# Kernel optimization log

Measured on AMD Instinct MI355X. Metric: run time of the kernel, lower is better.

## Reference

```python
import jax, jax.numpy as jnp
import numpy as np

N = 50000      # total nodes in batched graph
E = 800000     # total edges (avg degree 16)
B = 512        # number of graphs in batch
F_IN = 74      # input node feature size
H = 64         # hidden size per layer
OUT = 64       # output_feats
EPS = 1e-5     # BatchNorm eps


def setup_inputs() -> dict:
    key = jax.random.key(0)
    ks = jax.random.split(key, 32)
    d = {}
    d['feats'] = jax.random.normal(ks[0], (N, F_IN), dtype=jnp.float32)
    d['src'] = jax.random.randint(ks[1], (E,), 0, N)
    d['dst'] = jax.random.randint(ks[2], (E,), 0, N)
    d['graph_ids'] = jnp.sort(jax.random.randint(ks[3], (N,), 0, B))
    dims = [F_IN, H, H, H]
    i = 4
    for l in range(3):
        din, dout = dims[l], dims[l + 1]
        d[f'W{l}'] = jax.random.normal(ks[i], (din, dout), jnp.float32) / np.sqrt(din).astype(np.float32); i += 1
        d[f'b{l}'] = jnp.zeros((dout,), jnp.float32)
        d[f'rW{l}'] = jax.random.normal(ks[i], (din, dout), jnp.float32) / np.sqrt(din).astype(np.float32); i += 1
        d[f'rb{l}'] = jnp.zeros((dout,), jnp.float32)
        d[f'g{l}'] = jnp.ones((dout,), jnp.float32)    # BN gamma
        d[f'be{l}'] = jnp.zeros((dout,), jnp.float32)  # BN beta
    d['aw_W'] = jax.random.normal(ks[i], (H, 1), jnp.float32) / np.sqrt(H).astype(np.float32); i += 1
    d['aw_b'] = jnp.zeros((1,), jnp.float32)
    d['out_W'] = jax.random.normal(ks[i], (2 * H, OUT), jnp.float32) / np.sqrt(2 * H).astype(np.float32); i += 1
    d['out_b'] = jnp.zeros((OUT,), jnp.float32)
    return d


def _gcn_layer(x, src, dst, W, b, rW, rb, g, be):
    # GraphConv, norm='none': out = sum-aggregate(X W) + b, then relu
    xw = x @ W                                                    # [N, dout]
    agg = jax.ops.segment_sum(xw[src], dst, num_segments=N) + b   # gather/scatter over edges
    h = jax.nn.relu(agg)
    # residual: relu(Linear(x))
    h = h + jax.nn.relu(x @ rW + rb)
    # dropout p=0 -> identity
    # BatchNorm1d (training-mode batch statistics, biased variance)
    mean = jnp.mean(h, axis=0)
    var = jnp.var(h, axis=0)
    return (h - mean) * jax.lax.rsqrt(var + EPS) * g + be


def reference(feats, src, dst, graph_ids,
              W0, b0, rW0, rb0, g0, be0,
              W1, b1, rW1, rb1, g1, be1,
              W2, b2, rW2, rb2, g2, be2,
              aw_W, aw_b, out_W, out_b):
    h = feats
    h = _gcn_layer(h, src, dst, W0, b0, rW0, rb0, g0, be0)
    h = _gcn_layer(h, src, dst, W1, b1, rW1, rb1, g1, be1)
    h = _gcn_layer(h, src, dst, W2, b2, rW2, rb2, g2, be2)
    # WeightedSumAndMax readout
    w = jax.nn.sigmoid(h @ aw_W + aw_b)                               # [N, 1]
    h_sum = jax.ops.segment_sum(h * w, graph_ids, num_segments=B)     # [B, H]
    h_max = jax.ops.segment_max(h, graph_ids, num_segments=B)         # [B, H]
    h_max = jnp.where(jnp.isfinite(h_max), h_max, 0.0)                # empty graphs -> 0 (dgl max_nodes)
    h_g = jnp.concatenate([h_sum, h_max], axis=1)                     # [B, 2H]
    return h_g @ out_W + out_b                                        # [B, OUT]
```

## Files before the change

### kernel.cpp

```cpp
#include <hip/hip_runtime.h>
#include <hip/hip_bf16.h>
#include <math.h>

#define NN 50000
#define NE 800000
#define NB 512
#define FIN 74
#define HD 64
#define BN_EPS 1e-5f

#define CHUNK 32
#define ELLW 32
#define NBLK ((NN + CHUNK - 1) / CHUNK)
#define NBUCK2 NBLK
#define EB2 128
#define EPB (NE / EB2)
#define OCAPW 96


__global__ __launch_bounds__(256) void hist2_kernel(const int* __restrict__ dst,
                                                    int* __restrict__ H,
                                                    float* __restrict__ stats012,
                                                    unsigned long long* __restrict__ xw_zrow,
                                                    const float* __restrict__ W0,
                                                    const float* __restrict__ rW0,
                                                    float2* __restrict__ Wpk0) {
    __shared__ int lh[NBUCK2];
    int b = blockIdx.x, tid = threadIdx.x;
    for (int i = tid; i < NBUCK2; i += 256) lh[i] = 0;
    __syncthreads();
    int e0 = b * EPB;
    for (int i = tid; i < EPB; i += 256) atomicAdd(&lh[dst[e0 + i] >> 5], 1);
    if (b == 0) {
        for (int i = tid; i < 384; i += 256) stats012[i] = 0.f;
        if (tid < 16) xw_zrow[tid] = 0ull;
        for (int i = tid; i < FIN * HD; i += 256) Wpk0[i] = make_float2(W0[i], rW0[i]);
    }
    __syncthreads();
    for (int i = tid; i < NBUCK2; i += 256) H[b * NBUCK2 + i] = lh[i];
}

__global__ __launch_bounds__(128) void scanA2_kernel(int* __restrict__ H, int* __restrict__ T) {
    __shared__ int l[128];
    int k = blockIdx.x, tid = threadIdx.x;
    int v = H[tid * NBUCK2 + k];
    l[tid] = v;
    __syncthreads();
    for (int off = 1; off < 128; off <<= 1) {
        int t = (tid >= off) ? l[tid - off] : 0;
        __syncthreads();
        l[tid] += t;
        __syncthreads();
    }
    H[tid * NBUCK2 + k] = l[tid] - v;
    if (tid == 127) T[k] = l[127];
}

__global__ __launch_bounds__(256) void scanB2_kernel(const int* __restrict__ T,
                                                     int* __restrict__ bbase) {
    __shared__ int l[256];
    __shared__ int carry;
    int tid = threadIdx.x;
    if (tid == 0) carry = 0;
    __syncthreads();
    for (int c0 = 0; c0 < NBUCK2; c0 += 256) {
        int v = (c0 + tid < NBUCK2) ? T[c0 + tid] : 0;
        l[tid] = v;
        __syncthreads();
        for (int off = 1; off < 256; off <<= 1) {
            int t = (tid >= off) ? l[tid - off] : 0;
            __syncthreads();
            l[tid] += t;
            __syncthreads();
        }
        if (c0 + tid < NBUCK2) bbase[c0 + tid] = l[tid] - v + carry;
        __syncthreads();
        if (tid == 0) carry += l[255];
        __syncthreads();
    }
    if (tid == 0) bbase[NBUCK2] = carry;
}

__global__ __launch_bounds__(256) void scatter2_kernel(const int* __restrict__ src,
                                                       const int* __restrict__ dst,
                                                       const int* __restrict__ H,
                                                       const int* __restrict__ bbase,
                                                       unsigned* __restrict__ pairs) {
    __shared__ int cur[NBUCK2];
    int b = blockIdx.x, tid = threadIdx.x;
    for (int i = tid; i < NBUCK2; i += 256) cur[i] = H[b * NBUCK2 + i] + bbase[i];
    __syncthreads();
    int e0 = b * EPB;
    for (int i = tid; i < EPB; i += 256) {
        int d = dst[e0 + i];
        int s = src[e0 + i];
        int pos = atomicAdd(&cur[d >> 5], 1);
        pairs[pos] = (unsigned)s | ((unsigned)(d & 31) << 17);
    }
}


template <int K>
__global__ __launch_bounds__(256) void gemm_dual_kernel(
    const float* __restrict__ x, const float2* __restrict__ Wpk,
    const float* __restrict__ rb, __hip_bfloat16* __restrict__ xw,
    __hip_bfloat16* __restrict__ res, int n) {
    __shared__ float2 sW[K * HD];
    __shared__ float srb[64];
    for (int i = threadIdx.x; i < K * HD; i += 256) sW[i] = Wpk[i];
    if (threadIdx.x < 64) srb[threadIdx.x] = rb[threadIdx.x];
    __syncthreads();
    int wl = threadIdx.x >> 6, lane = threadIdx.x & 63;
    for (int r0 = (blockIdx.x * 4 + wl) * 8; r0 < n; r0 += gridDim.x * 32) {
        float a1[8], a2[8];
#pragma unroll
        for (int r = 0; r < 8; ++r) { a1[r] = 0.f; a2[r] = 0.f; }
#pragma unroll
        for (int c0 = 0; c0 < K; c0 += 64) {
            const int cl = (K - c0 < 64) ? (K - c0) : 64;
            float xv[8];
#pragma unroll
            for (int r = 0; r < 8; ++r) {
                int row = r0 + r;
                xv[r] = (lane < cl && row < n) ? x[(size_t)row * K + c0 + lane] : 0.f;
            }
            for (int j = 0; j < cl; ++j) {
                float2 w = sW[(c0 + j) * HD + lane];
#pragma unroll
                for (int r = 0; r < 8; ++r) {
                    float xb = __uint_as_float(
                        __builtin_amdgcn_readlane(__float_as_uint(xv[r]), j));
                    a1[r] = fmaf(xb, w.x, a1[r]);
                    a2[r] = fmaf(xb, w.y, a2[r]);
                }
            }
        }
#pragma unroll
        for (int r = 0; r < 8; ++r) {
            int row = r0 + r;
            if (row < n) {
                xw[(size_t)row * HD + lane] = __float2bfloat16(a1[r]);
                res[(size_t)row * HD + lane] = __float2bfloat16(fmaxf(a2[r] + srb[lane], 0.f));
            }
        }
    }
}

__global__ void fold_kernel(const float* __restrict__ stats, const float* __restrict__ g,
                            const float* __restrict__ be, const float* __restrict__ W,
                            const float* __restrict__ rW, const float* __restrict__ rb,
                            float2* __restrict__ Wpk, float* __restrict__ shiftW,
                            float* __restrict__ rbp) {
    __shared__ float sc[64], sh[64];
    int t = threadIdx.x;
    if (t < 64) {
        float mean = stats[t] / (float)NN;
        float var = stats[64 + t] / (float)NN - mean * mean;
        float scale = g[t] * rsqrtf(var + BN_EPS);
        sc[t] = scale;
        sh[t] = be[t] - mean * scale;
    }
    __syncthreads();
    for (int i = t; i < 64 * 64; i += 256) {
        int k = i >> 6;
        Wpk[i] = make_float2(sc[k] * W[i], sc[k] * rW[i]);
    }
    if (t < 64) {
        float sw = 0.f, srw = 0.f;
        for (int k = 0; k < 64; ++k) {
            sw = fmaf(sh[k], W[k * 64 + t], sw);
            srw = fmaf(sh[k], rW[k * 64 + t], srw);
        }
        shiftW[t] = sw;
        rbp[t] = rb[t] + srw;
    }
}

__device__ __forceinline__ float bf_lo(unsigned int p) { return __uint_as_float(p << 16); }
__device__ __forceinline__ float bf_hi(unsigned int p) { return __uint_as_float(p & 0xffff0000u); }

#define GATHER16(BASE)                                             \
    {                                                              \
        unsigned long long d[16];                                  \
        _Pragma("unroll") for (int j = 0; j < 16; ++j) {           \
            int idx = myIdx[(BASE) + j];                           \
            unsigned off = (unsigned)idx * 16u + (unsigned)c8;     \
            d[j] = XWu[off];                                       \
        }                                                          \
        _Pragma("unroll") for (int j = 0; j < 16; ++j) {           \
            unsigned lo = (unsigned)d[j], hi = (unsigned)(d[j] >> 32); \
            a0 += bf_lo(lo); a1 += bf_hi(lo);                      \
            a2 += bf_lo(hi); a3 += bf_hi(hi);                      \
        }                                                          \
    }

__global__ __launch_bounds__(256, 6) void fused_agg_kernel(
    const __hip_bfloat16* __restrict__ xw, const __hip_bfloat16* __restrict__ res,
    const float* __restrict__ b, const float* __restrict__ shiftW,
    const int* __restrict__ bbase, const unsigned* __restrict__ pairs,
    float* __restrict__ hout, float* __restrict__ stats, int n) {
    __shared__ int sIdx[4][8][ELLW + 1];
    __shared__ int sLen[4][8];
    __shared__ unsigned oflow[4][OCAPW];
    __shared__ int ocnt[4];
    __shared__ float lsr[4][16][8];

    int tid = threadIdx.x;
    int wl = tid >> 6, lane = tid & 63;
    int r0 = blockIdx.x * CHUNK;

    for (int i = lane; i < 8 * (ELLW + 1); i += 64) ((int*)sIdx[wl])[i] = NN;
    if (lane < 8) sLen[wl][lane] = 0;
    if (lane == 0) ocnt[wl] = 0;

    int beg = bbase[blockIdx.x], end = bbase[blockIdx.x + 1];
    for (int i = beg + lane; i < end; i += 64) {
        unsigned v = pairs[i];
        int rloc = (int)(v >> 17);
        if ((rloc >> 3) == wl) {
            int r8 = rloc & 7;
            int rk = atomicAdd(&sLen[wl][r8], 1);
            if (rk < ELLW) {
                sIdx[wl][r8][rk] = (int)(v & 0x1FFFFu);
            } else {
                int o = atomicAdd(&ocnt[wl], 1);
                if (o < OCAPW) oflow[wl][o] = v;
            }
        }
    }
    int nof = ocnt[wl];
    int noflow = (nof < OCAPW) ? nof : OCAPW;

    const unsigned long long* XWu = (const unsigned long long*)xw;
    const unsigned long long* REu = (const unsigned long long*)res;
    int q = lane >> 4, c8 = lane & 15;
    float4 bv = *(const float4*)&b[4 * c8];
    float4 swv = shiftW ? *(const float4*)&shiftW[4 * c8] : make_float4(0.f, 0.f, 0.f, 0.f);
    float s0 = 0.f, s1 = 0.f, s2 = 0.f, s3 = 0.f;
    float q0 = 0.f, q1 = 0.f, q2 = 0.f, q3 = 0.f;

#pragma unroll
    for (int p = 0; p < 2; ++p) {
        int r8 = p * 4 + q;
        int grow = r0 + wl * 8 + r8;
        int growc = (grow < n) ? grow : (n - 1);
        int l0 = sLen[wl][p * 4], l1 = sLen[wl][p * 4 + 1];
        int l2 = sLen[wl][p * 4 + 2], l3 = sLen[wl][p * 4 + 3];
        int m01 = (l0 > l1) ? l0 : l1, m23 = (l2 > l3) ? l2 : l3;
        int kmax = (m01 > m23) ? m01 : m23;
        int mylen = sLen[wl][r8];
        const int* myIdx = sIdx[wl][r8];
        unsigned long long rqw = REu[(unsigned)growc * 16u + (unsigned)c8];
        float a0 = 0.f, a1 = 0.f, a2 = 0.f, a3 = 0.f;
        GATHER16(0)
        if (kmax > 16) GATHER16(16)
        if (kmax > ELLW) {
            int myrloc = wl * 8 + r8;
            for (int o = 0; o < noflow; ++o) {
                unsigned v = oflow[wl][o];
                if ((int)(v >> 17) == myrloc) {
                    unsigned off = (v & 0x1FFFFu) * 16u + (unsigned)c8;
                    unsigned long long u = XWu[off];
                    unsigned lo = (unsigned)u, hi = (unsigned)(u >> 32);
                    a0 += bf_lo(lo); a1 += bf_hi(lo);
                    a2 += bf_lo(hi); a3 += bf_hi(hi);
                }
            }
        }
        unsigned rlo = (unsigned)rqw, rhi = (unsigned)(rqw >> 32);
        float dg = (float)mylen;
        float h0 = fmaxf(a0 + fmaf(dg, swv.x, bv.x), 0.f) + bf_lo(rlo);
        float h1 = fmaxf(a1 + fmaf(dg, swv.y, bv.y), 0.f) + bf_hi(rlo);
        float h2 = fmaxf(a2 + fmaf(dg, swv.z, bv.z), 0.f) + bf_lo(rhi);
        float h3 = fmaxf(a3 + fmaf(dg, swv.w, bv.w), 0.f) + bf_hi(rhi);
        if (grow < n) {
            *(float4*)&hout[(unsigned)grow * 64u + 4u * c8] = make_float4(h0, h1, h2, h3);
            s0 += h0; s1 += h1; s2 += h2; s3 += h3;
            q0 += h0 * h0; q1 += h1 * h1; q2 += h2 * h2; q3 += h3 * h3;
        }
    }

    s0 += __shfl_xor(s0, 16, 64); s0 += __shfl_xor(s0, 32, 64);
    s1 += __shfl_xor(s1, 16, 64); s1 += __shfl_xor(s1, 32, 64);
    s2 += __shfl_xor(s2, 16, 64); s2 += __shfl_xor(s2, 32, 64);
    s3 += __shfl_xor(s3, 16, 64); s3 += __shfl_xor(s3, 32, 64);
    q0 += __shfl_xor(q0, 16, 64); q0 += __shfl_xor(q0, 32, 64);
    q1 += __shfl_xor(q1, 16, 64); q1 += __shfl_xor(q1, 32, 64);
    q2 += __shfl_xor(q2, 16, 64); q2 += __shfl_xor(q2, 32, 64);
    q3 += __shfl_xor(q3, 16, 64); q3 += __shfl_xor(q3, 32, 64);
    if (q == 0) {
        lsr[wl][c8][0] = s0; lsr[wl][c8][1] = s1; lsr[wl][c8][2] = s2; lsr[wl][c8][3] = s3;
        lsr[wl][c8][4] = q0; lsr[wl][c8][5] = q1; lsr[wl][c8][6] = q2; lsr[wl][c8][7] = q3;
    }
    __syncthreads();
    if (tid < 64) {
        int c8i = tid >> 2, comp = tid & 3;
        float ssum = lsr[0][c8i][comp] + lsr[1][c8i][comp] + lsr[2][c8i][comp] + lsr[3][c8i][comp];
        float qsum = lsr[0][c8i][4 + comp] + lsr[1][c8i][4 + comp] + lsr[2][c8i][4 + comp] +
                     lsr[3][c8i][4 + comp];
        atomicAdd(&stats[tid], ssum);
        atomicAdd(&stats[64 + tid], qsum);
    }
}


__global__ void readout_init_kernel(float* __restrict__ hsum, unsigned int* __restrict__ hmax,
                                    const float* __restrict__ stats, const float* __restrict__ g,
                                    const float* __restrict__ be, float* __restrict__ ss) {
    int idx = blockIdx.x * 256 + threadIdx.x;
    if (idx < NB * HD) {
        hsum[idx] = 0.f;
        hmax[idx] = 0x007FFFFFu;
    }
    if (blockIdx.x == 0 && threadIdx.x < 64) {
        int c = threadIdx.x;
        float mean = stats[c] / (float)NN;
        float var = stats[64 + c] / (float)NN - mean * mean;
        float scale = g[c] * rsqrtf(var + BN_EPS);
        ss[c] = scale;
        ss[64 + c] = be[c] - mean * scale;
    }
}

#define RNODES 16

__device__ __forceinline__ void ro_flush(float* hsum, unsigned int* hmax, int g, int c,
                                         float accS, float accM) {
    atomicAdd(&hsum[g * HD + c], accS);
    unsigned int bits = __float_as_uint(accM);
    unsigned int enc = (bits & 0x80000000u) ? ~bits : (bits | 0x80000000u);
    atomicMax(&hmax[g * HD + c], enc);
}

__global__ __launch_bounds__(256) void readout_kernel(
    const float* __restrict__ h, const int* __restrict__ gid, const float* __restrict__ ss,
    const float* __restrict__ awW, const float* __restrict__ awb, float* __restrict__ hsum,
    unsigned int* __restrict__ hmax, int n) {
    int wid = blockIdx.x * 4 + (threadIdx.x >> 6);
    int c = threadIdx.x & 63;
    int r0 = wid * RNODES;
    if (r0 >= n) return;
    int r1 = r0 + RNODES;
    if (r1 > n) r1 = n;
    float aw = awW[c], ab = awb[0];
    float sA = ss[c], sB = ss[64 + c];
    int cur = gid[r0];
    float accS = 0.f, accM = -__builtin_inff();
    for (int r = r0; r < r1; ++r) {
        int g = gid[r];
        if (g != cur) {
            ro_flush(hsum, hmax, cur, c, accS, accM);
            accS = 0.f;
            accM = -__builtin_inff();
            cur = g;
        }
        float v = fmaf(h[(size_t)r * HD + c], sA, sB);
        float p = v * aw;
        for (int off = 32; off; off >>= 1) p += __shfl_xor(p, off, 64);
        float w = 1.f / (1.f + expf(-(p + ab)));
        accS = fmaf(v, w, accS);
        accM = fmaxf(accM, v);
    }
    ro_flush(hsum, hmax, cur, c, accS, accM);
}

__global__ void final_kernel(const float* __restrict__ hsum, const unsigned int* __restrict__ hmax,
                             const float* __restrict__ outW, const float* __restrict__ outb,
                             float* __restrict__ out) {
    __shared__ float sW[128 * 64];
    for (int i = threadIdx.x; i < 128 * 64; i += 256) sW[i] = outW[i];
    __syncthreads();
    int idx = blockIdx.x * 256 + threadIdx.x;
    if (idx >= NB * HD) return;
    int bi = idx >> 6, o = idx & 63;
    float acc = outb[o];
#pragma unroll 4
    for (int k = 0; k < 64; ++k) acc = fmaf(hsum[bi * 64 + k], sW[k * 64 + o], acc);
#pragma unroll 4
    for (int k = 0; k < 64; ++k) {
        unsigned int e = hmax[bi * 64 + k];
        float m;
        if (e == 0x007FFFFFu) {
            m = 0.f;
        } else {
            m = (e & 0x80000000u) ? __uint_as_float(e ^ 0x80000000u) : __uint_as_float(~e);
        }
        acc = fmaf(m, sW[(64 + k) * 64 + o], acc);
    }
    out[idx] = acc;
}


extern "C" void kernel_launch(void* const* d_in, const int* in_sizes, int n_in,
                              void* d_out, int out_size, void* d_ws, size_t ws_size,
                              hipStream_t stream) {
    const float* feats = (const float*)d_in[0];
    const int* src = (const int*)d_in[1];
    const int* dst = (const int*)d_in[2];
    const int* gid = (const int*)d_in[3];
    const float* W[3];
    const float* b[3];
    const float* rW[3];
    const float* rb[3];
    const float* g[3];
    const float* be[3];
    for (int l = 0; l < 3; ++l) {
        W[l] = (const float*)d_in[4 + 6 * l + 0];
        b[l] = (const float*)d_in[4 + 6 * l + 1];
        rW[l] = (const float*)d_in[4 + 6 * l + 2];
        rb[l] = (const float*)d_in[4 + 6 * l + 3];
        g[l] = (const float*)d_in[4 + 6 * l + 4];
        be[l] = (const float*)d_in[4 + 6 * l + 5];
    }
    const float* awW = (const float*)d_in[22];
    const float* awb = (const float*)d_in[23];
    const float* outW = (const float*)d_in[24];
    const float* outb = (const float*)d_in[25];
    float* out = (float*)d_out;

    __hip_bfloat16* XW = (__hip_bfloat16*)d_ws;
    __hip_bfloat16* RES = XW + (size_t)(NN + 1) * HD;
    float* P1 = (float*)(RES + (size_t)NN * HD);
    float* stats = P1 + (size_t)NN * HD;
    float* ss2 = stats + 384;
    float2* WPK = (float2*)(ss2 + 128);
    float* shW = (float*)(WPK + FIN * HD);
    float* rbp = shW + 64;
    float* hsum = rbp + 64;
    unsigned int* hmax = (unsigned int*)(hsum + (size_t)NB * HD);
    unsigned* pairs = (unsigned*)(hmax + (size_t)NB * HD);
    int* H = (int*)(pairs + (size_t)NE);
    int* T = H + (size_t)EB2 * NBUCK2;
    int* bbase = T + NBUCK2;

    float* stats0 = stats;
    float* stats1 = stats + 128;
    float* stats2 = stats + 256;

    const int GEMMBLK = 1280;
    const int ROBLK = (NN + RNODES * 4 - 1) / (RNODES * 4);

    hist2_kernel<<<EB2, 256, 0, stream>>>(dst, H, stats,
                                          (unsigned long long*)(XW + (size_t)NN * HD),
                                          W[0], rW[0], WPK);
    scanA2_kernel<<<NBUCK2, 128, 0, stream>>>(H, T);
    scanB2_kernel<<<1, 256, 0, stream>>>(T, bbase);
    scatter2_kernel<<<EB2, 256, 0, stream>>>(src, dst, H, bbase, pairs);

    gemm_dual_kernel<FIN><<<GEMMBLK, 256, 0, stream>>>(feats, WPK, rb[0], XW, RES, NN);
    fused_agg_kernel<<<NBLK, 256, 0, stream>>>(XW, RES, b[0], (const float*)nullptr, bbase,
                                               pairs, P1, stats0, NN);

    fold_kernel<<<1, 256, 0, stream>>>(stats0, g[0], be[0], W[1], rW[1], rb[1], WPK, shW, rbp);
    gemm_dual_kernel<HD><<<GEMMBLK, 256, 0, stream>>>(P1, WPK, rbp, XW, RES, NN);
    fused_agg_kernel<<<NBLK, 256, 0, stream>>>(XW, RES, b[1], shW, bbase, pairs, P1, stats1, NN);

    fold_kernel<<<1, 256, 0, stream>>>(stats1, g[1], be[1], W[2], rW[2], rb[2], WPK, shW, rbp);
    gemm_dual_kernel<HD><<<GEMMBLK, 256, 0, stream>>>(P1, WPK, rbp, XW, RES, NN);
    fused_agg_kernel<<<NBLK, 256, 0, stream>>>(XW, RES, b[2], shW, bbase, pairs, P1, stats2, NN);

    readout_init_kernel<<<(NB * HD + 255) / 256, 256, 0, stream>>>(hsum, hmax, stats2, g[2], be[2], ss2);
    readout_kernel<<<ROBLK, 256, 0, stream>>>(P1, gid, ss2, awW, awb, hsum, hmax, NN);
    final_kernel<<<(NB * HD + 255) / 256, 256, 0, stream>>>(hsum, hmax, outW, outb, out);
}
```

Baseline: 323.2 us.

## Precompute ELL adjacency once and split aggregation into two half-width passes

Measured after the change: 351.1 us. +8.6%, slower.

```diff
diff --git a/kernel.cpp b/kernel.cpp
--- a/kernel.cpp
+++ b/kernel.cpp
@@ -10,18 +10,18 @@
 #define BN_EPS 1e-5f
 
 #define CHUNK 32
-#define ELLW 32
+#define ELLW 48
 #define NBLK ((NN + CHUNK - 1) / CHUNK)
 #define NBUCK2 NBLK
 #define EB2 128
 #define EPB (NE / EB2)
-#define OCAPW 96
 
 
 __global__ __launch_bounds__(256) void hist2_kernel(const int* __restrict__ dst,
                                                     int* __restrict__ H,
                                                     float* __restrict__ stats012,
-                                                    unsigned long long* __restrict__ xw_zrow,
+                                                    unsigned long long* __restrict__ zlo,
+                                                    unsigned long long* __restrict__ zhi,
                                                     const float* __restrict__ W0,
                                                     const float* __restrict__ rW0,
                                                     float2* __restrict__ Wpk0) {
@@ -33,7 +33,7 @@
     for (int i = tid; i < EPB; i += 256) atomicAdd(&lh[dst[e0 + i] >> 5], 1);
     if (b == 0) {
         for (int i = tid; i < 384; i += 256) stats012[i] = 0.f;
-        if (tid < 16) xw_zrow[tid] = 0ull;
+        if (tid < 8) { zlo[tid] = 0ull; zhi[tid] = 0ull; }
         for (int i = tid; i < FIN * HD; i += 256) Wpk0[i] = make_float2(W0[i], rW0[i]);
     }
     __syncthreads();
@@ -99,18 +99,47 @@
     }
 }
 
+__global__ __launch_bounds__(256) void ellify_kernel(const unsigned* __restrict__ pairs,
+                                                     const int* __restrict__ bbase,
+                                                     int* __restrict__ ell,
+                                                     int* __restrict__ deg, int n) {
+    __shared__ int lcnt[CHUNK];
+    int bk = blockIdx.x, tid = threadIdx.x;
+    if (tid < CHUNK) lcnt[tid] = 0;
+    __syncthreads();
+    int beg = bbase[bk], end = bbase[bk + 1];
+    int r0 = bk * CHUNK;
+    for (int i = beg + tid; i < end; i += 256) {
+        unsigned v = pairs[i];
+        int rloc = (int)(v >> 17);
+        int rk = atomicAdd(&lcnt[rloc], 1);
+        if (rk < ELLW) ell[(size_t)(r0 + rloc) * ELLW + rk] = (int)(v & 0x1FFFFu);
+    }
+    __syncthreads();
+    for (int i = tid; i < CHUNK * ELLW; i += 256) {
+        int r = i / ELLW, j = i - r * ELLW;
+        if (r0 + r < n && j >= lcnt[r]) ell[(size_t)(r0 + r) * ELLW + j] = NN;
+    }
+    if (tid < CHUNK && r0 + tid < n) {
+        int d = lcnt[tid];
+        deg[r0 + tid] = (d < ELLW) ? d : ELLW;
+    }
+}
+
 
 template <int K>
 __global__ __launch_bounds__(256) void gemm_dual_kernel(
     const float* __restrict__ x, const float2* __restrict__ Wpk,
-    const float* __restrict__ rb, __hip_bfloat16* __restrict__ xw,
-    __hip_bfloat16* __restrict__ res, int n) {
+    const float* __restrict__ rb, __hip_bfloat16* __restrict__ xwlo,
+    __hip_bfloat16* __restrict__ xwhi, __hip_bfloat16* __restrict__ res, int n) {
     __shared__ float2 sW[K * HD];
     __shared__ float srb[64];
     for (int i = threadIdx.x; i < K * HD; i += 256) sW[i] = Wpk[i];
     if (threadIdx.x < 64) srb[threadIdx.x] = rb[threadIdx.x];
     __syncthreads();
     int wl = threadIdx.x >> 6, lane = threadIdx.x & 63;
+    __hip_bfloat16* xw = (lane < 32) ? xwlo : xwhi;
+    int cl32 = lane & 31;
     for (int r0 = (blockIdx.x * 4 + wl) * 8; r0 < n; r0 += gridDim.x * 32) {
         float a1[8], a2[8];
 #pragma unroll
@@ -139,7 +168,7 @@
         for (int r = 0; r < 8; ++r) {
             int row = r0 + r;
             if (row < n) {
-                xw[(size_t)row * HD + lane] = __float2bfloat16(a1[r]);
+                xw[(size_t)row * 32 + cl32] = __float2bfloat16(a1[r]);
                 res[(size_t)row * HD + lane] = __float2bfloat16(fmaxf(a2[r] + srb[lane], 0.f));
             }
         }
@@ -179,127 +208,80 @@
 __device__ __forceinline__ float bf_lo(unsigned int p) { return __uint_as_float(p << 16); }
 __device__ __forceinline__ float bf_hi(unsigned int p) { return __uint_as_float(p & 0xffff0000u); }
 
-#define GATHER16(BASE)                                             \
+#define GATH16(BASE)                                               \
     {                                                              \
-        unsigned long long d[16];                                  \
+        int id[16];                                                \
+        _Pragma("unroll") for (int j = 0; j < 16; ++j) id[j] = myIdx[(BASE) + j]; \
+        unsigned dd[16];                                           \
+        _Pragma("unroll") for (int j = 0; j < 16; ++j)             \
+            dd[j] = XWd[(unsigned)id[j] * 16u + (unsigned)c8];     \
         _Pragma("unroll") for (int j = 0; j < 16; ++j) {           \
-            int idx = myIdx[(BASE) + j];                           \
-            unsigned off = (unsigned)idx * 16u + (unsigned)c8;     \
-            d[j] = XWu[off];                                       \
+            a0 += bf_lo(dd[j]);                                    \
+            a1 += bf_hi(dd[j]);                                    \
         }                                                          \
-        _Pragma("unroll") for (int j = 0; j < 16; ++j) {           \
-            unsigned lo = (unsigned)d[j], hi = (unsigned)(d[j] >> 32); \
-            a0 += bf_lo(lo); a1 += bf_hi(lo);                      \
-            a2 += bf_lo(hi); a3 += bf_hi(hi);                      \
-        }                                                          \
-    }
-
-__global__ __launch_bounds__(256, 6) void fused_agg_kernel(
-    const __hip_bfloat16* __restrict__ xw, const __hip_bfloat16* __restrict__ res,
+    }
+
+template <int PHASE>
+__global__ __launch_bounds__(256) void agg_half_kernel(
+    const __hip_bfloat16* __restrict__ xwh, const __hip_bfloat16* __restrict__ res,
     const float* __restrict__ b, const float* __restrict__ shiftW,
-    const int* __restrict__ bbase, const unsigned* __restrict__ pairs,
+    const int* __restrict__ ell, const int* __restrict__ deg,
     float* __restrict__ hout, float* __restrict__ stats, int n) {
-    __shared__ int sIdx[4][8][ELLW + 1];
-    __shared__ int sLen[4][8];
-    __shared__ unsigned oflow[4][OCAPW];
-    __shared__ int ocnt[4];
-    __shared__ float lsr[4][16][8];
-
+    __shared__ float lsr[4][16][4];
     int tid = threadIdx.x;
     int wl = tid >> 6, lane = tid & 63;
+    int q = lane >> 4, c8 = lane & 15;
+    const unsigned* XWd = (const unsigned*)xwh;
+    const unsigned* REd = (const unsigned*)res;
     int r0 = blockIdx.x * CHUNK;
-
-    for (int i = lane; i < 8 * (ELLW + 1); i += 64) ((int*)sIdx[wl])[i] = NN;
-    if (lane < 8) sLen[wl][lane] = 0;
-    if (lane == 0) ocnt[wl] = 0;
-
-    int beg = bbase[blockIdx.x], end = bbase[blockIdx.x + 1];
-    for (int i = beg + lane; i < end; i += 64) {
-        unsigned v = pairs[i];
-        int rloc = (int)(v >> 17);
-        if ((rloc >> 3) == wl) {
-            int r8 = rloc & 7;
-            int rk = atomicAdd(&sLen[wl][r8], 1);
-            if (rk < ELLW) {
-                sIdx[wl][r8][rk] = (int)(v & 0x1FFFFu);
-            } else {
-                int o = atomicAdd(&ocnt[wl], 1);
-                if (o < OCAPW) oflow[wl][o] = v;
-            }
-        }
-    }
-    int nof = ocnt[wl];
-    int noflow = (nof < OCAPW) ? nof : OCAPW;
-
-    const unsigned long long* XWu = (const unsigned long long*)xw;
-    const unsigned long long* REu = (const unsigned long long*)res;
-    int q = lane >> 4, c8 = lane & 15;
-    float4 bv = *(const float4*)&b[4 * c8];
-    float4 swv = shiftW ? *(const float4*)&shiftW[4 * c8] : make_float4(0.f, 0.f, 0.f, 0.f);
-    float s0 = 0.f, s1 = 0.f, s2 = 0.f, s3 = 0.f;
-    float q0 = 0.f, q1 = 0.f, q2 = 0.f, q3 = 0.f;
+    float2 bv = *(const float2*)&b[PHASE * 32 + 2 * c8];
+    float2 swv = shiftW ? *(const float2*)&shiftW[PHASE * 32 + 2 * c8]
+                        : make_float2(0.f, 0.f);
+    float s0 = 0.f, s1 = 0.f, q0 = 0.f, q1 = 0.f;
 
 #pragma unroll
     for (int p = 0; p < 2; ++p) {
-        int r8 = p * 4 + q;
-        int grow = r0 + wl * 8 + r8;
+        int grow = r0 + wl * 8 + p * 4 + q;
         int growc = (grow < n) ? grow : (n - 1);
-        int l0 = sLen[wl][p * 4], l1 = sLen[wl][p * 4 + 1];
-        int l2 = sLen[wl][p * 4 + 2], l3 = sLen[wl][p * 4 + 3];
-        int m01 = (l0 > l1) ? l0 : l1, m23 = (l2 > l3) ? l2 : l3;
-        int kmax = (m01 > m23) ? m01 : m23;
-        int mylen = sLen[wl][r8];
-        const int* myIdx = sIdx[wl][r8];
-        unsigned long long rqw = REu[(unsigned)growc * 16u + (unsigned)c8];
-        float a0 = 0.f, a1 = 0.f, a2 = 0.f, a3 = 0.f;
-        GATHER16(0)
-        if (kmax > 16) GATHER16(16)
-        if (kmax > ELLW) {
-            int myrloc = wl * 8 + r8;
-            for (int o = 0; o < noflow; ++o) {
-                unsigned v = oflow[wl][o];
-                if ((int)(v >> 17) == myrloc) {
-                    unsigned off = (v & 0x1FFFFu) * 16u + (unsigned)c8;
-                    unsigned long long u = XWu[off];
-                    unsigned lo = (unsigned)u, hi = (unsigned)(u >> 32);
-                    a0 += bf_lo(lo); a1 += bf_hi(lo);
-                    a2 += bf_lo(hi); a3 += bf_hi(hi);
-                }
-            }
-        }
-        unsigned rlo = (unsigned)rqw, rhi = (unsigned)(rqw >> 32);
+        int mylen = (grow < n) ? deg[growc] : 0;
+        int kmax = mylen;
+        {
+            int t = __shfl_xor(kmax, 16, 64);
+            kmax = (t > kmax) ? t : kmax;
+            t = __shfl_xor(kmax, 32, 64);
+            kmax = (t > kmax) ? t : kmax;
+        }
+        const int* myIdx = &ell[(size_t)growc * ELLW];
+        unsigned rdw = REd[(unsigned)growc * 32u + (unsigned)(PHASE * 16 + c8)];
+        float a0 = 0.f, a1 = 0.f;
+        GATH16(0)
+        if (kmax > 16) GATH16(16)
+        if (kmax > 32) GATH16(32)
         float dg = (float)mylen;
-        float h0 = fmaxf(a0 + fmaf(dg, swv.x, bv.x), 0.f) + bf_lo(rlo);
-        float h1 = fmaxf(a1 + fmaf(dg, swv.y, bv.y), 0.f) + bf_hi(rlo);
-        float h2 = fmaxf(a2 + fmaf(dg, swv.z, bv.z), 0.f) + bf_lo(rhi);
-        float h3 = fmaxf(a3 + fmaf(dg, swv.w, bv.w), 0.f) + bf_hi(rhi);
+        float h0 = fmaxf(a0 + fmaf(dg, swv.x, bv.x), 0.f) + bf_lo(rdw);
+        float h1 = fmaxf(a1 + fmaf(dg, swv.y, bv.y), 0.f) + bf_hi(rdw);
         if (grow < n) {
-            *(float4*)&hout[(unsigned)grow * 64u + 4u * c8] = make_float4(h0, h1, h2, h3);
-            s0 += h0; s1 += h1; s2 += h2; s3 += h3;
-            q0 += h0 * h0; q1 += h1 * h1; q2 += h2 * h2; q3 += h3 * h3;
+            *(float2*)&hout[(unsigned)grow * 64u + (unsigned)(PHASE * 32 + 2 * c8)] =
+                make_float2(h0, h1);
+            s0 += h0; s1 += h1;
+            q0 += h0 * h0; q1 += h1 * h1;
         }
     }
 
     s0 += __shfl_xor(s0, 16, 64); s0 += __shfl_xor(s0, 32, 64);
     s1 += __shfl_xor(s1, 16, 64); s1 += __shfl_xor(s1, 32, 64);
-    s2 += __shfl_xor(s2, 16, 64); s2 += __shfl_xor(s2, 32, 64);
-    s3 += __shfl_xor(s3, 16, 64); s3 += __shfl_xor(s3, 32, 64);
     q0 += __shfl_xor(q0, 16, 64); q0 += __shfl_xor(q0, 32, 64);
     q1 += __shfl_xor(q1, 16, 64); q1 += __shfl_xor(q1, 32, 64);
-    q2 += __shfl_xor(q2, 16, 64); q2 += __shfl_xor(q2, 32, 64);
-    q3 += __shfl_xor(q3, 16, 64); q3 += __shfl_xor(q3, 32, 64);
     if (q == 0) {
-        lsr[wl][c8][0] = s0; lsr[wl][c8][1] = s1; lsr[wl][c8][2] = s2; lsr[wl][c8][3] = s3;
-        lsr[wl][c8][4] = q0; lsr[wl][c8][5] = q1; lsr[wl][c8][6] = q2; lsr[wl][c8][7] = q3;
+        lsr[wl][c8][0] = s0; lsr[wl][c8][1] = s1;
+        lsr[wl][c8][2] = q0; lsr[wl][c8][3] = q1;
     }
     __syncthreads();
     if (tid < 64) {
         int c8i = tid >> 2, comp = tid & 3;
-        float ssum = lsr[0][c8i][comp] + lsr[1][c8i][comp] + lsr[2][c8i][comp] + lsr[3][c8i][comp];
-        float qsum = lsr[0][c8i][4 + comp] + lsr[1][c8i][4 + comp] + lsr[2][c8i][4 + comp] +
-                     lsr[3][c8i][4 + comp];
-        atomicAdd(&stats[tid], ssum);
-        atomicAdd(&stats[64 + tid], qsum);
+        float v = lsr[0][c8i][comp] + lsr[1][c8i][comp] + lsr[2][c8i][comp] + lsr[3][c8i][comp];
+        int col = PHASE * 32 + 2 * c8i + (comp & 1);
+        atomicAdd(&stats[((comp >= 2) ? 64 : 0) + col], v);
     }
 }
 
@@ -418,8 +400,9 @@
     const float* outb = (const float*)d_in[25];
     float* out = (float*)d_out;
 
-    __hip_bfloat16* XW = (__hip_bfloat16*)d_ws;
-    __hip_bfloat16* RES = XW + (size_t)(NN + 1) * HD;
+    __hip_bfloat16* XWlo = (__hip_bfloat16*)d_ws;
+    __hip_bfloat16* XWhi = XWlo + (size_t)(NN + 1) * 32;
+    __hip_bfloat16* RES = XWhi + (size_t)(NN + 1) * 32;
     float* P1 = (float*)(RES + (size_t)NN * HD);
     float* stats = P1 + (size_t)NN * HD;
     float* ss2 = stats + 384;
@@ -432,6 +415,8 @@
     int* H = (int*)(pairs + (size_t)NE);
     int* T = H + (size_t)EB2 * NBUCK2;
     int* bbase = T + NBUCK2;
+    int* ell = bbase + NBUCK2 + 1;
+    int* deg = ell + (size_t)NN * ELLW;
 
     float* stats0 = stats;
     float* stats1 = stats + 128;
@@ -441,23 +426,29 @@
     const int ROBLK = (NN + RNODES * 4 - 1) / (RNODES * 4);
 
     hist2_kernel<<<EB2, 256, 0, stream>>>(dst, H, stats,
-                                          (unsigned long long*)(XW + (size_t)NN * HD),
+                                          (unsigned long long*)(XWlo + (size_t)NN * 32),
+                                          (unsigned long long*)(XWhi + (size_t)NN * 32),
                                           W[0], rW[0], WPK);
     scanA2_kernel<<<NBUCK2, 128, 0, stream>>>(H, T);
     scanB2_kernel<<<1, 256, 0, stream>>>(T, bbase);
     scatter2_kernel<<<EB2, 256, 0, stream>>>(src, dst, H, bbase, pairs);
-
-    gemm_dual_kernel<FIN><<<GEMMBLK, 256, 0, stream>>>(feats, WPK, rb[0], XW, RES, NN);
-    fused_agg_kernel<<<NBLK, 256, 0, stream>>>(XW, RES, b[0], (const float*)nullptr, bbase,
-                                               pairs, P1, stats0, NN);
+    ellify_kernel<<<NBUCK2, 256, 0, stream>>>(pairs, bbase, ell, deg, NN);
+
+    gemm_dual_kernel<FIN><<<GEMMBLK, 256, 0, stream>>>(feats, WPK, rb[0], XWlo, XWhi, RES, NN);
+    agg_half_kernel<0><<<NBLK, 256, 0, stream>>>(XWlo, RES, b[0], (const float*)nullptr, ell,
+                                                 deg, P1, stats0, NN);
+    agg_half_kernel<1><<<NBLK, 256, 0, stream>>>(XWhi, RES, b[0], (const float*)nullptr, ell,
+                                                 deg, P1, stats0, NN);
 
     fold_kernel<<<1, 256, 0, stream>>>(stats0, g[0], be[0], W[1], rW[1], rb[1], WPK, shW, rbp);
-    gemm_dual_kernel<HD><<<GEMMBLK, 256, 0, stream>>>(P1, WPK, rbp, XW, RES, NN);
-    fused_agg_kernel<<<NBLK, 256, 0, stream>>>(XW, RES, b[1], shW, bbase, pairs, P1, stats1, NN);
+    gemm_dual_kernel<HD><<<GEMMBLK, 256, 0, stream>>>(P1, WPK, rbp, XWlo, XWhi, RES, NN);
+    agg_half_kernel<0><<<NBLK, 256, 0, stream>>>(XWlo, RES, b[1], shW, ell, deg, P1, stats1, NN);
+    agg_half_kernel<1><<<NBLK, 256, 0, stream>>>(XWhi, RES, b[1], shW, ell, deg, P1, stats1, NN);
 
     fold_kernel<<<1, 256, 0, stream>>>(stats1, g[1], be[1], W[2], rW[2], rb[2], WPK, shW, rbp);
-    gemm_dual_kernel<HD><<<GEMMBLK, 256, 0, stream>>>(P1, WPK, rbp, XW, RES, NN);
-    fused_agg_kernel<<<NBLK, 256, 0, stream>>>(XW, RES, b[2], shW, bbase, pairs, P1, stats2, NN);
+    gemm_dual_kernel<HD><<<GEMMBLK, 256, 0, stream>>>(P1, WPK, rbp, XWlo, XWhi, RES, NN);
+    agg_half_kernel<0><<<NBLK, 256, 0, stream>>>(XWlo, RES, b[2], shW, ell, deg, P1, stats2, NN);
+    agg_half_kernel<1><<<NBLK, 256, 0, stream>>>(XWhi, RES, b[2], shW, ell, deg, P1, stats2, NN);
 
     readout_init_kernel<<<(NB * HD + 255) / 256, 256, 0, stream>>>(hsum, hmax, stats2, g[2], be[2], ss2);
     readout_kernel<<<ROBLK, 256, 0, stream>>>(P1, gid, ss2, awW, awb, hsum, hmax, NN);
```
